# Optimization experiments

Hardware: AMD Instinct MI355X
Metric: run time of the kernel (lower is better)

Reference implementation:

```python
import jax, jax.numpy as jnp
import numpy as np

NTOKENS = 500000
NSAMPLED = 8192
NHID = 256
BATCH = 8192


def setup_inputs() -> dict:
    key = jax.random.key(0)
    k1, k2, k3, k4, k5, k6, k7 = jax.random.split(key, 7)
    inputs = jax.random.normal(k1, (BATCH, NHID), dtype=jnp.float32)
    labels = jax.random.randint(k2, (BATCH,), 0, NTOKENS, dtype=jnp.int64)
    sample_ids = jax.random.randint(k3, (NSAMPLED,), 0, NTOKENS, dtype=jnp.int64)
    true_log_freq = jax.random.uniform(k4, (BATCH,), dtype=jnp.float32)
    sample_log_freq = jax.random.uniform(k5, (NSAMPLED,), dtype=jnp.float32)
    # Learned params: nn.Linear(nhid, ntokens) -> weight [ntokens, nhid], bias [ntokens]
    bound = 1.0 / np.sqrt(NHID)
    weight = jax.random.uniform(k6, (NTOKENS, NHID), dtype=jnp.float32, minval=-bound, maxval=bound)
    bias = jax.random.uniform(k7, (NTOKENS,), dtype=jnp.float32, minval=-bound, maxval=bound)
    return {
        "inputs": inputs,
        "labels": labels,
        "sample_ids": sample_ids,
        "true_log_freq": true_log_freq,
        "sample_log_freq": sample_log_freq,
        "weight": weight,
        "bias": bias,
    }


def reference(inputs, labels, sample_ids, true_log_freq, sample_log_freq, weight, bias):
    # Gather rows for true labels and sampled negatives
    true_weights = weight[labels]          # [B, nhid]
    true_bias = bias[labels]               # [B]
    sample_weights = weight[sample_ids]    # [S, nhid]
    sample_bias = bias[sample_ids]         # [S]

    # true logits: rowwise dot product + bias, minus log-freq correction
    true_logits = jnp.sum(inputs * true_weights, axis=1) + true_bias - true_log_freq  # [B]
    # sample logits: small GEMM against gathered rows, minus log-freq correction
    sample_logits = jnp.einsum("bd,sd->bs", inputs, sample_weights) + sample_bias - sample_log_freq  # [B, S]

    logits = jnp.concatenate([true_logits[:, None], sample_logits], axis=1)  # [B, 1+S]
    new_targets = jnp.zeros((inputs.shape[0],), dtype=jnp.int32)
    return logits, new_targets
```

## Files before the change

kernel.cpp:

```cpp
#include <hip/hip_runtime.h>
#include <hip/hip_bf16.h>

#define NTOKENS 500000
#define NSAMPLED 8192
#define NHID 256
#define BATCH 8192
#define LROW 8193
#define OUT_TAIL ((size_t)BATCH * LROW)

typedef short s16x8 __attribute__((ext_vector_type(8)));
typedef float f32x4 __attribute__((ext_vector_type(4)));
typedef unsigned short u16;

static __device__ __forceinline__ u16 f2bf(float f) {
  unsigned u = __float_as_uint(f);
  return (u16)((u + 0x7fffu + ((u >> 16) & 1u)) >> 16);
}

static __device__ __forceinline__ s16x8 pack8(float4 v0, float4 v1) {
  s16x8 o;
  o[0] = (short)f2bf(v0.x); o[1] = (short)f2bf(v0.y);
  o[2] = (short)f2bf(v0.z); o[3] = (short)f2bf(v0.w);
  o[4] = (short)f2bf(v1.x); o[5] = (short)f2bf(v1.y);
  o[6] = (short)f2bf(v1.z); o[7] = (short)f2bf(v1.w);
  return o;
}

static __device__ __forceinline__ void gload_lds16(const void* g, void* l) {
  __builtin_amdgcn_global_load_lds(
      (const __attribute__((address_space(1))) void*)g,
      (__attribute__((address_space(3))) void*)l, 16, 0, 0);
}

__global__ void k_prep(const float* __restrict__ inputs, const int* __restrict__ labels,
                       const int* __restrict__ sample_ids, const float* __restrict__ tfreq,
                       const float* __restrict__ sfreq, const float* __restrict__ weight,
                       const float* __restrict__ bias, u16* __restrict__ outA,
                       u16* __restrict__ outB, float* __restrict__ colconst,
                       float* __restrict__ out) {
  int bid = blockIdx.x;
  int t = threadIdx.x;
  if (bid < 1024) {
    size_t idx = ((size_t)bid * 256 + t) * 8;
    const float4* p = (const float4*)(inputs + idx);
    *(s16x8*)(outA + idx) = pack8(p[0], p[1]);
  } else if (bid < 2048) {
    int r = (bid - 1024) * 8 + (t >> 5);
    int l = t & 31;
    int s = sample_ids[r];
    const float* src = weight + (size_t)s * NHID + l * 8;
    *(s16x8*)(outB + (size_t)r * NHID + l * 8) =
        pack8(((const float4*)src)[0], ((const float4*)src)[1]);
    if (l == 0) colconst[r] = bias[s] - sfreq[r];
  } else {
    int bb = bid - 2048;
    int w = t >> 6, lane = t & 63;
    int b = bb * 4 + w;
    int lab = labels[b];
    const float4 x = *(const float4*)(inputs + (size_t)b * NHID + lane * 4);
    const float4 ww = *(const float4*)(weight + (size_t)lab * NHID + lane * 4);
    float s = x.x * ww.x + x.y * ww.y + x.z * ww.z + x.w * ww.w;
    #pragma unroll
    for (int off = 32; off; off >>= 1) s += __shfl_down(s, off, 64);
    if (lane == 0) out[(size_t)b * LROW] = s + bias[lab] - tfreq[b];
    int tid = bb * 256 + t;
    if (tid < BATCH) out[OUT_TAIL + tid] = 0.0f;
  }
}

__global__ __launch_bounds__(512, 4) void k_gemm(const u16* __restrict__ A,
                                                 const u16* __restrict__ B,
                                                 const float* __restrict__ colconst,
                                                 float* __restrict__ out) {
  __shared__ u16 lA[128 * 64];
  __shared__ u16 lB[256 * 64];
  int t = threadIdx.x;
  int lane = t & 63;
  int w = t >> 6;
  int bid = blockIdx.x;
  int brow = bid >> 5;
  int bcol = bid & 31;
  int wr = w >> 1, wc = w & 1;
  const int l15 = lane & 15;
  const int lhi = lane >> 4;

  f32x4 acc[2][8];
  #pragma unroll
  for (int a = 0; a < 2; ++a)
    #pragma unroll
    for (int b = 0; b < 8; ++b) acc[a][b] = (f32x4){0.f, 0.f, 0.f, 0.f};

  const u16* Abase = A + (size_t)brow * 128 * NHID;
  const u16* Bbase = B + (size_t)bcol * 256 * NHID;

  for (int kt = 0; kt < 4; ++kt) {
    #pragma unroll
    for (int j = 0; j < 2; ++j) {
      int chunk = w * 128 + j * 64 + lane;
      int row = chunk >> 3;
      int cs = (chunk & 7) ^ (row & 7);
      gload_lds16(Abase + (size_t)row * NHID + kt * 64 + cs * 8,
                  lA + (size_t)(w * 128 + j * 64) * 8);
    }
    #pragma unroll
    for (int j = 0; j < 4; ++j) {
      int chunk = w * 256 + j * 64 + lane;
      int row = chunk >> 3;
      int cs = (chunk & 7) ^ (row & 7);
      gload_lds16(Bbase + (size_t)row * NHID + kt * 64 + cs * 8,
                  lB + (size_t)(w * 256 + j * 64) * 8);
    }
    __syncthreads();
    #pragma unroll
    for (int ks = 0; ks < 2; ++ks) {
      int kc = ks * 4 + lhi;
      s16x8 af[2];
      #pragma unroll
      for (int mi = 0; mi < 2; ++mi) {
        int row = wr * 32 + mi * 16 + l15;
        af[mi] = *(const s16x8*)(lA + row * 64 + ((kc ^ (row & 7)) * 8));
      }
      #pragma unroll
      for (int ni = 0; ni < 8; ++ni) {
        int row = wc * 128 + ni * 16 + l15;
        s16x8 bf = *(const s16x8*)(lB + row * 64 + ((kc ^ (row & 7)) * 8));
        #pragma unroll
        for (int mi = 0; mi < 2; ++mi)
          acc[mi][ni] = __builtin_amdgcn_mfma_f32_16x16x32_bf16(af[mi], bf, acc[mi][ni], 0, 0, 0);
      }
    }
    __syncthreads();
  }

  int grow0 = brow * 128 + wr * 32;
  int gcol0 = bcol * 256 + wc * 128;
  float cc[8];
  #pragma unroll
  for (int ni = 0; ni < 8; ++ni) cc[ni] = colconst[gcol0 + ni * 16 + l15];
  #pragma unroll
  for (int mi = 0; mi < 2; ++mi) {
    #pragma unroll
    for (int r = 0; r < 4; ++r) {
      size_t rbase = (size_t)(grow0 + mi * 16 + lhi * 4 + r) * LROW + 1;
      #pragma unroll
      for (int ni = 0; ni < 8; ++ni)
        out[rbase + gcol0 + ni * 16 + l15] = acc[mi][ni][r] + cc[ni];
    }
  }
}

extern "C" void kernel_launch(void* const* d_in, const int* in_sizes, int n_in,
                              void* d_out, int out_size, void* d_ws, size_t ws_size,
                              hipStream_t stream) {
  const float* inputs          = (const float*)d_in[0];
  const int*   labels          = (const int*)d_in[1];
  const int*   sample_ids      = (const int*)d_in[2];
  const float* true_log_freq   = (const float*)d_in[3];
  const float* sample_log_freq = (const float*)d_in[4];
  const float* weight          = (const float*)d_in[5];
  const float* bias            = (const float*)d_in[6];
  float* out = (float*)d_out;

  u16* wsA = (u16*)d_ws;
  u16* wsB = wsA + (size_t)BATCH * NHID;
  float* colconst = (float*)(wsB + (size_t)NSAMPLED * NHID);

  hipLaunchKernelGGL(k_prep, dim3(4096), dim3(256), 0, stream,
                     inputs, labels, sample_ids, true_log_freq, sample_log_freq,
                     weight, bias, wsA, wsB, colconst, out);
  hipLaunchKernelGGL(k_gemm, dim3(2048), dim3(512), 0, stream, wsA, wsB, colconst, out);
}
```

Before: 86.23 us.

## Double-buffer GEMM LDS tiles with K=32 stages to overlap loads and MFMA

Splits the K loop into eight 32-wide stages and double-buffers A/B tiles in LDS, issuing the async global-to-LDS load for the next stage before computing on the current one. This replaces the two barriers per 64-wide step with a single barrier per stage and uses a new paired-row swizzle to keep LDS reads conflict-free. LDS footprint stays the same, but there are twice as many iterations and smaller load batches. The kernel is likely bound by the large output store, so the gain may be small.

```diff
diff --git a/kernel.cpp b/kernel.cpp
--- a/kernel.cpp
+++ b/kernel.cpp
@@ -72,8 +72,8 @@
                                                  const u16* __restrict__ B,
                                                  const float* __restrict__ colconst,
                                                  float* __restrict__ out) {
-  __shared__ u16 lA[128 * 64];
-  __shared__ u16 lB[256 * 64];
+  __shared__ u16 lA[2][128 * 32];
+  __shared__ u16 lB[2][256 * 32];
   int t = threadIdx.x;
   int lane = t & 63;
   int w = t >> 6;
@@ -93,43 +93,49 @@
   const u16* Abase = A + (size_t)brow * 128 * NHID;
   const u16* Bbase = B + (size_t)bcol * 256 * NHID;
 
-  for (int kt = 0; kt < 4; ++kt) {
+  auto stage = [&](int buf, int kt) {
+    {
+      int idx = w * 64 + lane;
+      int rp = idx >> 3, cp = (idx & 7) ^ (rp & 7);
+      int row = rp * 2 + (cp >> 2), c = cp & 3;
+      gload_lds16(Abase + (size_t)row * NHID + kt * 32 + c * 8,
+                  &lA[buf][(size_t)(w * 64) * 8]);
+    }
     #pragma unroll
     for (int j = 0; j < 2; ++j) {
-      int chunk = w * 128 + j * 64 + lane;
-      int row = chunk >> 3;
-      int cs = (chunk & 7) ^ (row & 7);
-      gload_lds16(Abase + (size_t)row * NHID + kt * 64 + cs * 8,
-                  lA + (size_t)(w * 128 + j * 64) * 8);
+      int idx = (w * 2 + j) * 64 + lane;
+      int rp = idx >> 3, cp = (idx & 7) ^ (rp & 7);
+      int row = rp * 2 + (cp >> 2), c = cp & 3;
+      gload_lds16(Bbase + (size_t)row * NHID + kt * 32 + c * 8,
+                  &lB[buf][(size_t)((w * 2 + j) * 64) * 8]);
+    }
+  };
+
+  stage(0, 0);
+  __syncthreads();
+  int cur = 0;
+  for (int kt = 0; kt < 8; ++kt) {
+    if (kt < 7) stage(cur ^ 1, kt + 1);
+    s16x8 af[2];
+    #pragma unroll
+    for (int mi = 0; mi < 2; ++mi) {
+      int ra = wr * 32 + mi * 16 + l15;
+      int rp = ra >> 1;
+      int slot = (((ra & 1) << 2) | lhi) ^ (rp & 7);
+      af[mi] = *(const s16x8*)(&lA[cur][rp * 64 + slot * 8]);
     }
     #pragma unroll
-    for (int j = 0; j < 4; ++j) {
-      int chunk = w * 256 + j * 64 + lane;
-      int row = chunk >> 3;
-      int cs = (chunk & 7) ^ (row & 7);
-      gload_lds16(Bbase + (size_t)row * NHID + kt * 64 + cs * 8,
-                  lB + (size_t)(w * 256 + j * 64) * 8);
+    for (int ni = 0; ni < 8; ++ni) {
+      int rb = wc * 128 + ni * 16 + l15;
+      int rp = rb >> 1;
+      int slot = (((rb & 1) << 2) | lhi) ^ (rp & 7);
+      s16x8 bf = *(const s16x8*)(&lB[cur][rp * 64 + slot * 8]);
+      #pragma unroll
+      for (int mi = 0; mi < 2; ++mi)
+        acc[mi][ni] = __builtin_amdgcn_mfma_f32_16x16x32_bf16(af[mi], bf, acc[mi][ni], 0, 0, 0);
     }
     __syncthreads();
-    #pragma unroll
-    for (int ks = 0; ks < 2; ++ks) {
-      int kc = ks * 4 + lhi;
-      s16x8 af[2];
-      #pragma unroll
-      for (int mi = 0; mi < 2; ++mi) {
-        int row = wr * 32 + mi * 16 + l15;
-        af[mi] = *(const s16x8*)(lA + row * 64 + ((kc ^ (row & 7)) * 8));
-      }
-      #pragma unroll
-      for (int ni = 0; ni < 8; ++ni) {
-        int row = wc * 128 + ni * 16 + l15;
-        s16x8 bf = *(const s16x8*)(lB + row * 64 + ((kc ^ (row & 7)) * 8));
-        #pragma unroll
-        for (int mi = 0; mi < 2; ++mi)
-          acc[mi][ni] = __builtin_amdgcn_mfma_f32_16x16x32_bf16(af[mi], bf, acc[mi][ni], 0, 0, 0);
-      }
-    }
-    __syncthreads();
+    cur ^= 1;
   }
 
   int grow0 = brow * 128 + wr * 32;
```

Measured after the change: 88.99 us. 3.2% more time.
